# Kernel optimization log

Measured on AMD Instinct MI355X. Metric: run time of the kernel, lower is better.

## Reference

```python
import jax, jax.numpy as jnp
import numpy as np

H = 32  # hidden size (hard-coded in the torch module)


def lstm_forward(x, W_ih, W_hh, b_ih, b_hh):
    """Single-layer unidirectional LSTM, batch_first. PyTorch gate order i,f,g,o.
    x: [B,S,3] -> hs: [B,S,H]"""
    B = x.shape[0]
    b = b_ih + b_hh  # fuse the two biases
    # precompute input projections for all timesteps: [B,S,4H]
    xg = jnp.einsum('bsi,gi->bsg', x, W_ih) + b

    def step(carry, xt):
        h, c = carry
        g = xt + h @ W_hh.T  # [B,4H]
        i = jax.nn.sigmoid(g[:, 0 * H:1 * H])
        f = jax.nn.sigmoid(g[:, 1 * H:2 * H])
        gg = jnp.tanh(g[:, 2 * H:3 * H])
        o = jax.nn.sigmoid(g[:, 3 * H:4 * H])
        c = f * c + i * gg
        h = o * jnp.tanh(c)
        return (h, c), h

    h0 = jnp.zeros((B, H), dtype=x.dtype)
    c0 = jnp.zeros((B, H), dtype=x.dtype)
    (_, _), hs = jax.lax.scan(step, (h0, c0), jnp.swapaxes(xg, 0, 1))  # scan over S
    return jnp.swapaxes(hs, 0, 1)  # [B,S,H]


def setup_inputs() -> dict:
    key = jax.random.key(0)
    ks = jax.random.split(key, 10)
    B, S, I, OUT = 2048, 1024, 3, 2
    s = 1.0 / np.sqrt(H)
    u = lambda k, shape: jax.random.uniform(k, shape, jnp.float32, -s, s)
    return {
        'x': jax.random.normal(ks[0], (B, S, I), jnp.float32),
        'W_ih': u(ks[1], (4 * H, I)),
        'W_hh': u(ks[2], (4 * H, H)),
        'b_ih': u(ks[3], (4 * H,)),
        'b_hh': u(ks[4], (4 * H,)),
        'attn_w': u(ks[5], (H, 1)),
        'fc1_w': u(ks[6], (16, H)),
        'fc1_b': u(ks[7], (16,)),
        'fc2_w': u(ks[8], (OUT, 16)),
        'fc2_b': u(ks[9], (OUT,)),
    }


def reference(x, W_ih, W_hh, b_ih, b_hh, attn_w, fc1_w, fc1_b, fc2_w, fc2_b):
    hs = lstm_forward(x, W_ih, W_hh, b_ih, b_hh)          # [B,S,H]
    scores = jnp.einsum('bsh,ho->bs', hs, attn_w)          # bmm with [H,1] weight
    attn = jax.nn.softmax(jax.nn.relu(scores), axis=-1)    # [B,S]
    pooled = jnp.einsum('bsh,bs->bh', hs, attn)            # weighted sum over S
    h1 = jax.nn.relu(pooled @ fc1_w.T + fc1_b)             # [B,16]
    return h1 @ fc2_w.T + fc2_b                            # [B,OUT]
```

## Files before the change

kernel.cpp:

```cpp
#include <hip/hip_runtime.h>

#define HSZ 32
#define SEQ 1024

typedef float v2f __attribute__((ext_vector_type(2)));

__device__ __forceinline__ float fast_rcp(float v) { return __builtin_amdgcn_rcpf(v); }

__device__ __forceinline__ float sigmoidf_(float v) {
    return fast_rcp(1.0f + __expf(-v));
}
__device__ __forceinline__ float tanhf_(float v) {
    return fmaf(2.0f, sigmoidf_(2.0f * v), -1.0f);
}

__global__ __launch_bounds__(64)
__attribute__((amdgpu_waves_per_eu(1, 1)))
void lstm_attn_fused(const float* __restrict__ x,
                     const float* __restrict__ W_ih,
                     const float* __restrict__ W_hh,
                     const float* __restrict__ b_ih,
                     const float* __restrict__ b_hh,
                     const float* __restrict__ attn_w,
                     const float* __restrict__ fc1_w,
                     const float* __restrict__ fc1_b,
                     const float* __restrict__ fc2_w,
                     const float* __restrict__ fc2_b,
                     float* __restrict__ out)
{
    const int lane = threadIdx.x;
    const int half = lane >> 5;
    const int u    = lane & 31;
    const int bsel = blockIdx.x * 2 + half;

    const v2f* __restrict__ Whv = (const v2f*)W_hh;
    const v2f* __restrict__ awp = (const v2f*)attn_w;
    v2f wI[16], wF[16], wG[16], wO[16], awv[16];
#pragma unroll
    for (int k = 0; k < 16; ++k) {
        wI[k]  = Whv[(u      ) * 16 + k];
        wF[k]  = Whv[(u + 32 ) * 16 + k];
        wG[k]  = Whv[(u + 64 ) * 16 + k];
        wO[k]  = Whv[(u + 96 ) * 16 + k];
        awv[k] = awp[k];
    }
    float wiI[3], wiF[3], wiG[3], wiO[3];
#pragma unroll
    for (int j = 0; j < 3; ++j) {
        wiI[j] = W_ih[(u      ) * 3 + j];
        wiF[j] = W_ih[(u + 32 ) * 3 + j];
        wiG[j] = W_ih[(u + 64 ) * 3 + j];
        wiO[j] = W_ih[(u + 96 ) * 3 + j];
    }
    float bI = b_ih[u     ] + b_hh[u     ];
    float bF = b_ih[u + 32] + b_hh[u + 32];
    float bG = b_ih[u + 64] + b_hh[u + 64];
    float bO = b_ih[u + 96] + b_hh[u + 96];

#pragma unroll
    for (int k = 0; k < 16; ++k) {
        asm volatile("" : "+v"(wI[k]), "+v"(wF[k]), "+v"(wG[k]), "+v"(wO[k]), "+v"(awv[k]));
    }
#pragma unroll
    for (int j = 0; j < 3; ++j) {
        asm volatile("" : "+v"(wiI[j]), "+v"(wiF[j]), "+v"(wiG[j]), "+v"(wiO[j]));
    }
    asm volatile("" : "+v"(bI), "+v"(bF), "+v"(bG), "+v"(bO));

    __shared__ float4 hbuf4[16];
    float* __restrict__ hbuf = (float*)hbuf4;
    hbuf[lane] = 0.0f;
    __syncthreads();

    float c = 0.0f, h = 0.0f;
    float Pacc = 0.0f, lacc = 0.0f;

    const float4* __restrict__ xv = (const float4*)(x + (size_t)bsel * SEQ * 3);

    auto ldh = [&](v2f hp[16]) {
        const float4* __restrict__ hb = hbuf4 + (half << 3);
        const float4 q0 = hb[0], q1 = hb[1], q2 = hb[2], q3 = hb[3];
        const float4 q4 = hb[4], q5 = hb[5], q6 = hb[6], q7 = hb[7];
        hp[0]={q0.x,q0.y}; hp[1]={q0.z,q0.w}; hp[2]={q1.x,q1.y}; hp[3]={q1.z,q1.w};
        hp[4]={q2.x,q2.y}; hp[5]={q2.z,q2.w}; hp[6]={q3.x,q3.y}; hp[7]={q3.z,q3.w};
        hp[8]={q4.x,q4.y}; hp[9]={q4.z,q4.w}; hp[10]={q5.x,q5.y}; hp[11]={q5.z,q5.w};
        hp[12]={q6.x,q6.y}; hp[13]={q6.z,q6.w}; hp[14]={q7.x,q7.y}; hp[15]={q7.z,q7.w};
    };

    auto step = [&](float x0, float x1, float x2, float accum) {
        v2f hp[16]; ldh(hp);

        v2f aI; aI.x = fmaf(wiI[0],x0, fmaf(wiI[1],x1, fmaf(wiI[2],x2, bI))); aI.y = 0.0f;
        v2f aF; aF.x = fmaf(wiF[0],x0, fmaf(wiF[1],x1, fmaf(wiF[2],x2, bF))); aF.y = 0.0f;
        v2f aG; aG.x = fmaf(wiG[0],x0, fmaf(wiG[1],x1, fmaf(wiG[2],x2, bG))); aG.y = 0.0f;
        v2f aO; aO.x = fmaf(wiO[0],x0, fmaf(wiO[1],x1, fmaf(wiO[2],x2, bO))); aO.y = 0.0f;
        v2f ap; ap.x = 0.0f; ap.y = 0.0f;
#pragma unroll
        for (int k = 0; k < 16; ++k) {
            aI = __builtin_elementwise_fma(wI[k],  hp[k], aI);
            aF = __builtin_elementwise_fma(wF[k],  hp[k], aF);
            aG = __builtin_elementwise_fma(wG[k],  hp[k], aG);
            aO = __builtin_elementwise_fma(wO[k],  hp[k], aO);
            ap = __builtin_elementwise_fma(awv[k], hp[k], ap);
        }

        const float p   = ap.x + ap.y;
        const float wgt = accum * __expf(fmaxf(p, 0.0f));
        lacc += wgt;
        Pacc = fmaf(wgt, h, Pacc);

        const float i_ = sigmoidf_(aI.x + aI.y);
        const float f_ = sigmoidf_(aF.x + aF.y);
        const float gg = tanhf_   (aG.x + aG.y);
        const float o_ = sigmoidf_(aO.x + aO.y);

        c = fmaf(f_, c, i_ * gg);
        h = o_ * tanhf_(c);

        __syncthreads();
        hbuf[lane] = h;
        __syncthreads();
    };

    float4 xa = xv[0], xb = xv[1], xc = xv[2];
    for (int s0 = 0; s0 < SEQ; s0 += 4) {
        const int nfi = ((s0 + 4) < SEQ) ? (((s0 + 4) * 3) >> 2) : 0;
        const float4 na = xv[nfi], nb = xv[nfi + 1], nc = xv[nfi + 2];
        step(xa.x, xa.y, xa.z, (s0 == 0) ? 0.0f : 1.0f);
        step(xa.w, xb.x, xb.y, 1.0f);
        step(xb.z, xb.w, xc.x, 1.0f);
        step(xc.y, xc.z, xc.w, 1.0f);
        xa = na; xb = nb; xc = nc;
    }
    {
        v2f hp[16]; ldh(hp);
        v2f ap; ap.x = 0.0f; ap.y = 0.0f;
#pragma unroll
        for (int k = 0; k < 16; ++k)
            ap = __builtin_elementwise_fma(awv[k], hp[k], ap);
        const float p   = ap.x + ap.y;
        const float wgt = __expf(fmaxf(p, 0.0f));
        lacc += wgt;
        Pacc = fmaf(wgt, h, Pacc);
    }

    __syncthreads();
    hbuf[lane] = Pacc / lacc;
    __syncthreads();

    float h1 = 0.0f;
    {
        const int j = lane & 15;
        const float* __restrict__ hb = hbuf + (half << 5);
        float acc = fc1_b[j];
#pragma unroll
        for (int k = 0; k < HSZ; ++k)
            acc = fmaf(fc1_w[j * HSZ + k], hb[k], acc);
        h1 = fmaxf(acc, 0.0f);
    }
    __shared__ float h1sh[2][16];
    if ((lane & 31) < 16) h1sh[half][lane & 15] = h1;
    __syncthreads();
    if ((lane & 31) < 2) {
        const int oi = lane & 31;
        float acc = fc2_b[oi];
#pragma unroll
        for (int m = 0; m < 16; ++m)
            acc = fmaf(fc2_w[oi * 16 + m], h1sh[half][m], acc);
        out[bsel * 2 + oi] = acc;
    }
}

extern "C" void kernel_launch(void* const* d_in, const int* in_sizes, int n_in,
                              void* d_out, int out_size, void* d_ws, size_t ws_size,
                              hipStream_t stream) {
    const float* x      = (const float*)d_in[0];
    const float* W_ih   = (const float*)d_in[1];
    const float* W_hh   = (const float*)d_in[2];
    const float* b_ih   = (const float*)d_in[3];
    const float* b_hh   = (const float*)d_in[4];
    const float* attn_w = (const float*)d_in[5];
    const float* fc1_w  = (const float*)d_in[6];
    const float* fc1_b  = (const float*)d_in[7];
    const float* fc2_w  = (const float*)d_in[8];
    const float* fc2_b  = (const float*)d_in[9];

    const int B = in_sizes[0] / (SEQ * 3);

    lstm_attn_fused<<<dim3(B / 2), dim3(64), 0, stream>>>(
        x, W_ih, W_hh, b_ih, b_hh, attn_w, fc1_w, fc1_b, fc2_w, fc2_b,
        (float*)d_out);
}
```

Measured before the change: 340.6 us.

## Drop per-step barriers and compute attention score via cross-lane swizzle reduction

Each block is a single 64-lane wavefront, so the two __syncthreads around the per-step hidden-state exchange are removed, on the assumption that in-order LDS access within one wave is enough. The attention score is now computed once per step from the new h: each lane multiplies its h by its attention weight, and ds_swizzle xor steps sum the products across the 32 lanes. This replaces the 16 extra packed FMAs per lane over the loaded hidden vector, frees the 32 registers that held the attention weights, and removes the epilogue step. The waves-per-EU hint is raised from 1 to 2. The change risks adding swizzle latency to each step and relies on wave-synchronous memory ordering.

```diff
diff --git a/kernel.cpp b/kernel.cpp
--- a/kernel.cpp
+++ b/kernel.cpp
@@ -14,8 +14,12 @@
     return fmaf(2.0f, sigmoidf_(2.0f * v), -1.0f);
 }
 
+__device__ __forceinline__ float swz_add(float v, const int imm) {
+    return v;
+}
+
 __global__ __launch_bounds__(64)
-__attribute__((amdgpu_waves_per_eu(1, 1)))
+__attribute__((amdgpu_waves_per_eu(2, 2)))
 void lstm_attn_fused(const float* __restrict__ x,
                      const float* __restrict__ W_ih,
                      const float* __restrict__ W_hh,
@@ -34,15 +38,13 @@
     const int bsel = blockIdx.x * 2 + half;
 
     const v2f* __restrict__ Whv = (const v2f*)W_hh;
-    const v2f* __restrict__ awp = (const v2f*)attn_w;
-    v2f wI[16], wF[16], wG[16], wO[16], awv[16];
+    v2f wI[16], wF[16], wG[16], wO[16];
 #pragma unroll
     for (int k = 0; k < 16; ++k) {
-        wI[k]  = Whv[(u      ) * 16 + k];
-        wF[k]  = Whv[(u + 32 ) * 16 + k];
-        wG[k]  = Whv[(u + 64 ) * 16 + k];
-        wO[k]  = Whv[(u + 96 ) * 16 + k];
-        awv[k] = awp[k];
+        wI[k] = Whv[(u      ) * 16 + k];
+        wF[k] = Whv[(u + 32 ) * 16 + k];
+        wG[k] = Whv[(u + 64 ) * 16 + k];
+        wO[k] = Whv[(u + 96 ) * 16 + k];
     }
     float wiI[3], wiF[3], wiG[3], wiO[3];
 #pragma unroll
@@ -56,58 +58,43 @@
     float bF = b_ih[u + 32] + b_hh[u + 32];
     float bG = b_ih[u + 64] + b_hh[u + 64];
     float bO = b_ih[u + 96] + b_hh[u + 96];
+    float aw = attn_w[u];
 
 #pragma unroll
     for (int k = 0; k < 16; ++k) {
-        asm volatile("" : "+v"(wI[k]), "+v"(wF[k]), "+v"(wG[k]), "+v"(wO[k]), "+v"(awv[k]));
+        asm volatile("" : "+v"(wI[k]), "+v"(wF[k]), "+v"(wG[k]), "+v"(wO[k]));
     }
 #pragma unroll
     for (int j = 0; j < 3; ++j) {
         asm volatile("" : "+v"(wiI[j]), "+v"(wiF[j]), "+v"(wiG[j]), "+v"(wiO[j]));
     }
-    asm volatile("" : "+v"(bI), "+v"(bF), "+v"(bG), "+v"(bO));
+    asm volatile("" : "+v"(bI), "+v"(bF), "+v"(bG), "+v"(bO), "+v"(aw));
 
-    __shared__ float4 hbuf4[16];
-    float* __restrict__ hbuf = (float*)hbuf4;
+    __shared__ float hbuf[64];
     hbuf[lane] = 0.0f;
-    __syncthreads();
 
     float c = 0.0f, h = 0.0f;
     float Pacc = 0.0f, lacc = 0.0f;
 
     const float4* __restrict__ xv = (const float4*)(x + (size_t)bsel * SEQ * 3);
+    const v2f* __restrict__ hb2 = (const v2f*)hbuf + (half << 4);
 
-    auto ldh = [&](v2f hp[16]) {
-        const float4* __restrict__ hb = hbuf4 + (half << 3);
-        const float4 q0 = hb[0], q1 = hb[1], q2 = hb[2], q3 = hb[3];
-        const float4 q4 = hb[4], q5 = hb[5], q6 = hb[6], q7 = hb[7];
-        hp[0]={q0.x,q0.y}; hp[1]={q0.z,q0.w}; hp[2]={q1.x,q1.y}; hp[3]={q1.z,q1.w};
-        hp[4]={q2.x,q2.y}; hp[5]={q2.z,q2.w}; hp[6]={q3.x,q3.y}; hp[7]={q3.z,q3.w};
-        hp[8]={q4.x,q4.y}; hp[9]={q4.z,q4.w}; hp[10]={q5.x,q5.y}; hp[11]={q5.z,q5.w};
-        hp[12]={q6.x,q6.y}; hp[13]={q6.z,q6.w}; hp[14]={q7.x,q7.y}; hp[15]={q7.z,q7.w};
-    };
-
-    auto step = [&](float x0, float x1, float x2, float accum) {
-        v2f hp[16]; ldh(hp);
+    auto step = [&](float x0, float x1, float x2) {
+        v2f hp[16];
+#pragma unroll
+        for (int k = 0; k < 16; ++k) hp[k] = hb2[k];
 
         v2f aI; aI.x = fmaf(wiI[0],x0, fmaf(wiI[1],x1, fmaf(wiI[2],x2, bI))); aI.y = 0.0f;
         v2f aF; aF.x = fmaf(wiF[0],x0, fmaf(wiF[1],x1, fmaf(wiF[2],x2, bF))); aF.y = 0.0f;
         v2f aG; aG.x = fmaf(wiG[0],x0, fmaf(wiG[1],x1, fmaf(wiG[2],x2, bG))); aG.y = 0.0f;
         v2f aO; aO.x = fmaf(wiO[0],x0, fmaf(wiO[1],x1, fmaf(wiO[2],x2, bO))); aO.y = 0.0f;
-        v2f ap; ap.x = 0.0f; ap.y = 0.0f;
 #pragma unroll
         for (int k = 0; k < 16; ++k) {
-            aI = __builtin_elementwise_fma(wI[k],  hp[k], aI);
-            aF = __builtin_elementwise_fma(wF[k],  hp[k], aF);
-            aG = __builtin_elementwise_fma(wG[k],  hp[k], aG);
-            aO = __builtin_elementwise_fma(wO[k],  hp[k], aO);
-            ap = __builtin_elementwise_fma(awv[k], hp[k], ap);
+            aI = __builtin_elementwise_fma(wI[k], hp[k], aI);
+            aF = __builtin_elementwise_fma(wF[k], hp[k], aF);
+            aG = __builtin_elementwise_fma(wG[k], hp[k], aG);
+            aO = __builtin_elementwise_fma(wO[k], hp[k], aO);
         }
-
-        const float p   = ap.x + ap.y;
-        const float wgt = accum * __expf(fmaxf(p, 0.0f));
-        lacc += wgt;
-        Pacc = fmaf(wgt, h, Pacc);
 
         const float i_ = sigmoidf_(aI.x + aI.y);
         const float f_ = sigmoidf_(aF.x + aF.y);
@@ -117,38 +104,32 @@
         c = fmaf(f_, c, i_ * gg);
         h = o_ * tanhf_(c);
 
-        __syncthreads();
         hbuf[lane] = h;
-        __syncthreads();
+
+        float p = h * aw;
+        p += __int_as_float(__builtin_amdgcn_ds_swizzle(__float_as_int(p), 0x041F));
+        p += __int_as_float(__builtin_amdgcn_ds_swizzle(__float_as_int(p), 0x081F));
+        p += __int_as_float(__builtin_amdgcn_ds_swizzle(__float_as_int(p), 0x101F));
+        p += __int_as_float(__builtin_amdgcn_ds_swizzle(__float_as_int(p), 0x201F));
+        p += __int_as_float(__builtin_amdgcn_ds_swizzle(__float_as_int(p), 0x401F));
+        const float wgt = __expf(fmaxf(p, 0.0f));
+        lacc += wgt;
+        Pacc = fmaf(wgt, h, Pacc);
     };
 
     float4 xa = xv[0], xb = xv[1], xc = xv[2];
     for (int s0 = 0; s0 < SEQ; s0 += 4) {
         const int nfi = ((s0 + 4) < SEQ) ? (((s0 + 4) * 3) >> 2) : 0;
         const float4 na = xv[nfi], nb = xv[nfi + 1], nc = xv[nfi + 2];
-        step(xa.x, xa.y, xa.z, (s0 == 0) ? 0.0f : 1.0f);
-        step(xa.w, xb.x, xb.y, 1.0f);
-        step(xb.z, xb.w, xc.x, 1.0f);
-        step(xc.y, xc.z, xc.w, 1.0f);
+        step(xa.x, xa.y, xa.z);
+        step(xa.w, xb.x, xb.y);
+        step(xb.z, xb.w, xc.x);
+        step(xc.y, xc.z, xc.w);
         xa = na; xb = nb; xc = nc;
     }
-    {
-        v2f hp[16]; ldh(hp);
-        v2f ap; ap.x = 0.0f; ap.y = 0.0f;
-#pragma unroll
-        for (int k = 0; k < 16; ++k)
-            ap = __builtin_elementwise_fma(awv[k], hp[k], ap);
-        const float p   = ap.x + ap.y;
-        const float wgt = __expf(fmaxf(p, 0.0f));
-        lacc += wgt;
-        Pacc = fmaf(wgt, h, Pacc);
-    }
 
-    __syncthreads();
-    hbuf[lane] = Pacc / lacc;
-    __syncthreads();
+    hbuf[lane] = Pacc * fast_rcp(lacc);
 
-    float h1 = 0.0f;
     {
         const int j = lane & 15;
         const float* __restrict__ hb = hbuf + (half << 5);
@@ -156,18 +137,17 @@
 #pragma unroll
         for (int k = 0; k < HSZ; ++k)
             acc = fmaf(fc1_w[j * HSZ + k], hb[k], acc);
-        h1 = fmaxf(acc, 0.0f);
-    }
-    __shared__ float h1sh[2][16];
-    if ((lane & 31) < 16) h1sh[half][lane & 15] = h1;
-    __syncthreads();
-    if ((lane & 31) < 2) {
-        const int oi = lane & 31;
-        float acc = fc2_b[oi];
+        __shared__ float h1sh[2][16];
+        if ((lane & 31) < 16) h1sh[half][j] = fmaxf(acc, 0.0f);
+
+        if ((lane & 31) < 2) {
+            const int oi = lane & 31;
+            float acc2 = fc2_b[oi];
 #pragma unroll
-        for (int m = 0; m < 16; ++m)
-            acc = fmaf(fc2_w[oi * 16 + m], h1sh[half][m], acc);
-        out[bsel * 2 + oi] = acc;
+            for (int m = 0; m < 16; ++m)
+                acc2 = fmaf(fc2_w[oi * 16 + m], h1sh[half][m], acc2);
+            out[bsel * 2 + oi] = acc2;
+        }
     }
 }
 
```

New measurement: 353.6 us. +3.8%, slower.
